# Kernel optimization log

Hardware: AMD Instinct MI355X
Metric: run time of the kernel (lower is better)

The kernel has to match this reference:

```python
import jax, jax.numpy as jnp
import numpy as np

B, D, F = 32768, 512, 512  # batch, input features, output features (num_feats)


def setup_inputs() -> dict:
    key = jax.random.key(0)
    kx, kw, ka, kb = jax.random.split(key, 4)
    x = jax.random.normal(kx, (B, D), dtype=jnp.float32)
    W = jax.random.normal(kw, (F, D), dtype=jnp.float32) / np.float32(np.sqrt(D))
    a = jax.random.normal(ka, (F,), dtype=jnp.float32)
    b = jax.random.normal(kb, (F,), dtype=jnp.float32)
    return {"x": x, "W": W, "a": a, "b": b}


def reference(x, W, a, b):
    # Vectorized form of the nested map_fn:
    # out[i, f] = tanh(b[f] + a[f] * dot(W[f, :], x[i, :]))
    z = jnp.einsum('bd,fd->bf', x, W)  # [B, F] GEMM replacing per-(sample,feature) dots
    return jnp.tanh(a * z + b)
```

## Files before the change

### kernel.cpp

```cpp
#include <hip/hip_runtime.h>
#include <hip/hip_bf16.h>
#include <math.h>


typedef short        bf16x8 __attribute__((ext_vector_type(8)));
typedef float        f32x4  __attribute__((ext_vector_type(4)));
typedef unsigned int u32x2  __attribute__((ext_vector_type(2)));

static constexpr int Mdim = 32768;
static constexpr int Kdim = 512;
static constexpr int Ndim = 512;

__device__ __forceinline__ unsigned cvt_pk_bf16(float a, float b) {
  unsigned r;
  asm("v_cvt_pk_bf16_f32 %0, %1, %2" : "=v"(r) : "v"(a), "v"(b));
  return r;
}

__device__ __forceinline__ void split4(f32x4 v, u32x2& hi, u32x2& lo) {
  unsigned h0 = cvt_pk_bf16(v[0], v[1]);
  unsigned h1 = cvt_pk_bf16(v[2], v[3]);
  float f0 = __uint_as_float(h0 << 16);
  float f1 = __uint_as_float(h0 & 0xFFFF0000u);
  float f2 = __uint_as_float(h1 << 16);
  float f3 = __uint_as_float(h1 & 0xFFFF0000u);
  lo[0] = cvt_pk_bf16(v[0] - f0, v[1] - f1);
  lo[1] = cvt_pk_bf16(v[2] - f2, v[3] - f3);
  hi[0] = h0; hi[1] = h1;
}

__device__ __forceinline__ float fast_tanh(float x) {
  float e = __expf(2.0f * x);
  return 1.0f - 2.0f * __builtin_amdgcn_rcpf(e + 1.0f);
}

__global__ __launch_bounds__(512, 4) void gemm_split_tanh(
    const float* __restrict__ X, const float* __restrict__ Wm,
    const float* __restrict__ avec, const float* __restrict__ bvec,
    float* __restrict__ out) {
  __shared__ unsigned short lds[4][128 * 64];

  const int bid = blockIdx.x;
  const int nB  = bid & 3;
  const int mB  = bid >> 2;
  const int tid  = threadIdx.x;
  const int lane = tid & 63;
  const int wid  = tid >> 6;
  const int wm = wid >> 2, wn = wid & 3;

  f32x4 acc[4][2];
#pragma unroll
  for (int i = 0; i < 4; ++i)
#pragma unroll
    for (int j = 0; j < 2; ++j) acc[i][j] = {0.f, 0.f, 0.f, 0.f};

  const int srow  = tid >> 4;
  const int scol4 = tid & 15;
  const int kcol  = scol4 * 4;
  const int soff0 = ((kcol >> 3)) ;
  const float* Xb = X  + (size_t)mB * 128 * Kdim;
  const float* Wb = Wm + (size_t)nB * 128 * Kdim;

  f32x4 rA[4], rB[4];
#pragma unroll
  for (int i = 0; i < 4; ++i) {
    const int row = srow + 32 * i;
    rA[i] = *(const f32x4*)(Xb + (size_t)row * Kdim + kcol);
    rB[i] = *(const f32x4*)(Wb + (size_t)row * Kdim + kcol);
  }

  for (int kt = 0; kt < Kdim / 64; ++kt) {
#pragma unroll
    for (int i = 0; i < 4; ++i) {
      const int row = srow + 32 * i;
      const int off = row * 64 + (((soff0) ^ (row & 7)) << 3) + (kcol & 7);
      u32x2 h, l;
      split4(rA[i], h, l);
      *(u32x2*)&lds[0][off] = h;
      *(u32x2*)&lds[1][off] = l;
      split4(rB[i], h, l);
      *(u32x2*)&lds[2][off] = h;
      *(u32x2*)&lds[3][off] = l;
    }
    __syncthreads();

    if (kt != Kdim / 64 - 1) {
      const int kbase = (kt + 1) * 64;
#pragma unroll
      for (int i = 0; i < 4; ++i) {
        const int row = srow + 32 * i;
        rA[i] = *(const f32x4*)(Xb + (size_t)row * Kdim + kbase + kcol);
        rB[i] = *(const f32x4*)(Wb + (size_t)row * Kdim + kbase + kcol);
      }
    }

#pragma unroll
    for (int ks = 0; ks < 2; ++ks) {
      const int slotBase = ks * 4 + (lane >> 4);
      bf16x8 bh[2], bl[2];
#pragma unroll
      for (int ni = 0; ni < 2; ++ni) {
        const int row = wn * 32 + ni * 16 + (lane & 15);
        const int off = row * 64 + ((slotBase ^ (row & 7)) << 3);
        bh[ni] = *(const bf16x8*)&lds[2][off];
        bl[ni] = *(const bf16x8*)&lds[3][off];
      }
#pragma unroll
      for (int mi = 0; mi < 4; ++mi) {
        const int row = wm * 64 + mi * 16 + (lane & 15);
        const int off = row * 64 + ((slotBase ^ (row & 7)) << 3);
        bf16x8 ah = *(const bf16x8*)&lds[0][off];
        bf16x8 al = *(const bf16x8*)&lds[1][off];
#pragma unroll
        for (int ni = 0; ni < 2; ++ni) {
          acc[mi][ni] = __builtin_amdgcn_mfma_f32_16x16x32_bf16(ah, bh[ni], acc[mi][ni], 0, 0, 0);
          acc[mi][ni] = __builtin_amdgcn_mfma_f32_16x16x32_bf16(ah, bl[ni], acc[mi][ni], 0, 0, 0);
          acc[mi][ni] = __builtin_amdgcn_mfma_f32_16x16x32_bf16(al, bh[ni], acc[mi][ni], 0, 0, 0);
        }
      }
    }
    __syncthreads();
  }

  const int c  = lane & 15;
  const int rq = (lane >> 4) * 4;
#pragma unroll
  for (int ni = 0; ni < 2; ++ni) {
    const int gc = nB * 128 + wn * 32 + ni * 16 + c;
    const float aa = avec[gc];
    const float bb = bvec[gc];
#pragma unroll
    for (int mi = 0; mi < 4; ++mi) {
      const int gr = mB * 128 + wm * 64 + mi * 16 + rq;
      f32x4 v = acc[mi][ni];
#pragma unroll
      for (int j = 0; j < 4; ++j) {
        out[(size_t)(gr + j) * Ndim + gc] = fast_tanh(aa * v[j] + bb);
      }
    }
  }
}

extern "C" void kernel_launch(void* const* d_in, const int* in_sizes, int n_in,
                              void* d_out, int out_size, void* d_ws, size_t ws_size,
                              hipStream_t stream) {
  const float* X  = (const float*)d_in[0];
  const float* Wm = (const float*)d_in[1];
  const float* av = (const float*)d_in[2];
  const float* bv = (const float*)d_in[3];
  float* out = (float*)d_out;
  dim3 grid((Mdim / 128) * (Ndim / 128));
  dim3 block(512);
  gemm_split_tanh<<<grid, block, 0, stream>>>(X, Wm, av, bv, out);
}
```

Measured before the change: 157.9 us.

## Pre-split W into bf16 hi/lo workspace and stream it via global_load_lds

```diff
diff --git a/kernel.cpp b/kernel.cpp
--- a/kernel.cpp
+++ b/kernel.cpp
@@ -34,12 +34,144 @@
   return 1.0f - 2.0f * __builtin_amdgcn_rcpf(e + 1.0f);
 }
 
-__global__ __launch_bounds__(512, 4) void gemm_split_tanh(
+__device__ __forceinline__ void glds16(const unsigned short* g, unsigned short* l) {
+  __builtin_amdgcn_global_load_lds(
+      (const __attribute__((address_space(1))) unsigned int*)g,
+      (__attribute__((address_space(3))) unsigned int*)l, 16, 0, 0);
+}
+
+__global__ __launch_bounds__(256) void split_w(const float* __restrict__ Wm,
+                                               unsigned short* __restrict__ whi,
+                                               unsigned short* __restrict__ wlo) {
+  const int idx = blockIdx.x * 256 + threadIdx.x;
+  f32x4 v = *(const f32x4*)(Wm + (size_t)idx * 4);
+  u32x2 h, l;
+  split4(v, h, l);
+  *(u32x2*)(whi + (size_t)idx * 4) = h;
+  *(u32x2*)(wlo + (size_t)idx * 4) = l;
+}
+
+__global__ __launch_bounds__(512, 4) void gemm_ws(
+    const float* __restrict__ X,
+    const unsigned short* __restrict__ Whi, const unsigned short* __restrict__ Wlo,
+    const float* __restrict__ avec, const float* __restrict__ bvec,
+    float* __restrict__ out) {
+  __shared__ unsigned short lds[4][128 * 64];
+
+  const int bid = blockIdx.x;
+  const int vid = (bid & 7) * 128 + (bid >> 3);
+  const int nB  = vid & 3;
+  const int mB  = vid >> 2;
+  const int tid  = threadIdx.x;
+  const int lane = tid & 63;
+  const int wid  = tid >> 6;
+  const int wm = wid >> 2, wn = wid & 3;
+
+  f32x4 acc[4][2];
+#pragma unroll
+  for (int i = 0; i < 4; ++i)
+#pragma unroll
+    for (int j = 0; j < 2; ++j) acc[i][j] = {0.f, 0.f, 0.f, 0.f};
+
+  const int srow  = tid >> 4;
+  const int scol4 = tid & 15;
+  const int kcol  = scol4 * 4;
+  const int soff0 = kcol >> 3;
+  const float* Xb = X + (size_t)mB * 128 * Kdim;
+
+  const int rl = lane >> 3;
+  const int ssl = (lane & 7) ^ rl;
+  const int brow0 = nB * 128 + wid * 16 + rl;
+  const int brow1 = brow0 + 8;
+  const unsigned short* srcBhi0 = Whi + (size_t)brow0 * Kdim + ssl * 8;
+  const unsigned short* srcBhi1 = Whi + (size_t)brow1 * Kdim + ssl * 8;
+  const unsigned short* srcBlo0 = Wlo + (size_t)brow0 * Kdim + ssl * 8;
+  const unsigned short* srcBlo1 = Wlo + (size_t)brow1 * Kdim + ssl * 8;
+  unsigned short* dstB0 = &lds[0][(wid * 2 + 0) * 512];
+  unsigned short* dstB1 = &lds[0][(wid * 2 + 1) * 512];
+  const int planeSz = 128 * 64;
+
+  f32x4 rA[4];
+#pragma unroll
+  for (int i = 0; i < 4; ++i)
+    rA[i] = *(const f32x4*)(Xb + (size_t)(srow + 32 * i) * Kdim + kcol);
+
+  for (int kt = 0; kt < Kdim / 64; ++kt) {
+    const int kb = kt * 64;
+    glds16(srcBhi0 + kb, dstB0 + 2 * planeSz);
+    glds16(srcBhi1 + kb, dstB1 + 2 * planeSz);
+    glds16(srcBlo0 + kb, dstB0 + 3 * planeSz);
+    glds16(srcBlo1 + kb, dstB1 + 3 * planeSz);
+
+#pragma unroll
+    for (int i = 0; i < 4; ++i) {
+      const int row = srow + 32 * i;
+      const int off = row * 64 + ((soff0 ^ (row & 7)) << 3) + (kcol & 7);
+      u32x2 h, l;
+      split4(rA[i], h, l);
+      *(u32x2*)&lds[0][off] = h;
+      *(u32x2*)&lds[1][off] = l;
+    }
+    __syncthreads();
+
+    if (kt != Kdim / 64 - 1) {
+#pragma unroll
+      for (int i = 0; i < 4; ++i)
+        rA[i] = *(const f32x4*)(Xb + (size_t)(srow + 32 * i) * Kdim + kb + 64 + kcol);
+    }
+
+#pragma unroll
+    for (int ks = 0; ks < 2; ++ks) {
+      const int slotBase = ks * 4 + (lane >> 4);
+      bf16x8 bh[2], bl[2];
+#pragma unroll
+      for (int ni = 0; ni < 2; ++ni) {
+        const int row = wn * 32 + ni * 16 + (lane & 15);
+        const int off = row * 64 + ((slotBase ^ (row & 7)) << 3);
+        bh[ni] = *(const bf16x8*)&lds[2][off];
+        bl[ni] = *(const bf16x8*)&lds[3][off];
+      }
+#pragma unroll
+      for (int mi = 0; mi < 4; ++mi) {
+        const int row = wm * 64 + mi * 16 + (lane & 15);
+        const int off = row * 64 + ((slotBase ^ (row & 7)) << 3);
+        bf16x8 ah = *(const bf16x8*)&lds[0][off];
+        bf16x8 al = *(const bf16x8*)&lds[1][off];
+#pragma unroll
+        for (int ni = 0; ni < 2; ++ni) {
+          acc[mi][ni] = __builtin_amdgcn_mfma_f32_16x16x32_bf16(ah, bh[ni], acc[mi][ni], 0, 0, 0);
+          acc[mi][ni] = __builtin_amdgcn_mfma_f32_16x16x32_bf16(ah, bl[ni], acc[mi][ni], 0, 0, 0);
+          acc[mi][ni] = __builtin_amdgcn_mfma_f32_16x16x32_bf16(al, bh[ni], acc[mi][ni], 0, 0, 0);
+        }
+      }
+    }
+    __syncthreads();
+  }
+
+  const int c  = lane & 15;
+  const int rq = (lane >> 4) * 4;
+#pragma unroll
+  for (int ni = 0; ni < 2; ++ni) {
+    const int gc = nB * 128 + wn * 32 + ni * 16 + c;
+    const float aa = avec[gc];
+    const float bb = bvec[gc];
+#pragma unroll
+    for (int mi = 0; mi < 4; ++mi) {
+      const int gr = mB * 128 + wm * 64 + mi * 16 + rq;
+      f32x4 v = acc[mi][ni];
+#pragma unroll
+      for (int j = 0; j < 4; ++j) {
+        out[(size_t)(gr + j) * Ndim + gc] = fast_tanh(aa * v[j] + bb);
+      }
+    }
+  }
+}
+
+__global__ __launch_bounds__(512, 4) void gemm_nows(
     const float* __restrict__ X, const float* __restrict__ Wm,
     const float* __restrict__ avec, const float* __restrict__ bvec,
     float* __restrict__ out) {
   __shared__ unsigned short lds[4][128 * 64];
-
   const int bid = blockIdx.x;
   const int nB  = bid & 3;
   const int mB  = bid >> 2;
@@ -57,7 +189,7 @@
   const int srow  = tid >> 4;
   const int scol4 = tid & 15;
   const int kcol  = scol4 * 4;
-  const int soff0 = ((kcol >> 3)) ;
+  const int soff0 = kcol >> 3;
   const float* Xb = X  + (size_t)mB * 128 * Kdim;
   const float* Wb = Wm + (size_t)nB * 128 * Kdim;
 
@@ -73,7 +205,7 @@
 #pragma unroll
     for (int i = 0; i < 4; ++i) {
       const int row = srow + 32 * i;
-      const int off = row * 64 + (((soff0) ^ (row & 7)) << 3) + (kcol & 7);
+      const int off = row * 64 + ((soff0 ^ (row & 7)) << 3) + (kcol & 7);
       u32x2 h, l;
       split4(rA[i], h, l);
       *(u32x2*)&lds[0][off] = h;
@@ -83,7 +215,6 @@
       *(u32x2*)&lds[3][off] = l;
     }
     __syncthreads();
-
     if (kt != Kdim / 64 - 1) {
       const int kbase = (kt + 1) * 64;
 #pragma unroll
@@ -93,7 +224,6 @@
         rB[i] = *(const f32x4*)(Wb + (size_t)row * Kdim + kbase + kcol);
       }
     }
-
 #pragma unroll
     for (int ks = 0; ks < 2; ++ks) {
       const int slotBase = ks * 4 + (lane >> 4);
@@ -149,7 +279,14 @@
   const float* av = (const float*)d_in[2];
   const float* bv = (const float*)d_in[3];
   float* out = (float*)d_out;
-  dim3 grid((Mdim / 128) * (Ndim / 128));
-  dim3 block(512);
-  gemm_split_tanh<<<grid, block, 0, stream>>>(X, Wm, av, bv, out);
-}
+
+  const size_t wSplitBytes = (size_t)Ndim * Kdim * 2 * sizeof(unsigned short);
+  if (ws_size >= wSplitBytes) {
+    unsigned short* whi = (unsigned short*)d_ws;
+    unsigned short* wlo = whi + (size_t)Ndim * Kdim;
+    split_w<<<dim3(Ndim * Kdim / 4 / 256), dim3(256), 0, stream>>>(Wm, whi, wlo);
+    gemm_ws<<<dim3((Mdim / 128) * (Ndim / 128)), dim3(512), 0, stream>>>(X, whi, wlo, av, bv, out);
+  } else {
+    gemm_nows<<<dim3((Mdim / 128) * (Ndim / 128)), dim3(512), 0, stream>>>(X, Wm, av, bv, out);
+  }
+}
```

Result: no change. 158.0 us (+0.1%).
